# Optimization experiments

Measured on AMD Instinct MI355X. Metric: run time of the kernel, lower is better.

The kernel has to match this reference:

```python
import jax, jax.numpy as jnp
import numpy as np

BRIGHT_THRESH = 0.65
SAT_THRESH = 0.15
SMOOTH_K = 15
LAMBDA_L1 = 1.0
LAMBDA_WIN_L1 = 3.0
LAMBDA_WIN_COLOR = 1.0
WINDOW_WEIGHT = 5.0
BASE_WEIGHT = 1.0
TRANSFORM_WEIGHT = 2.0
EPS = 1e-8


def _avg_pool_same(x, k=SMOOTH_K):
    # AvgPool2d(k, stride=1, padding=k//2), count_include_pad=True (torch default)
    p = k // 2
    s = jax.lax.reduce_window(x, 0.0, jax.lax.add, (1, 1, k, k), (1, 1, 1, 1),
                              [(0, 0), (0, 0), (p, p), (p, p)])
    return s / (k * k)


def _window_detector(source):
    # Rescale from [-1,1] to [0,1] if any negative values present
    src = jnp.where(source.min() < 0, (source + 1) * 0.5, source)
    brightness = 0.299 * src[:, 0:1] + 0.587 * src[:, 1:2] + 0.114 * src[:, 2:3]
    bright_mask = jax.nn.sigmoid(20.0 * (brightness - BRIGHT_THRESH))
    saturation = src.max(axis=1, keepdims=True) - src.min(axis=1, keepdims=True)
    low_sat_mask = jax.nn.sigmoid(20.0 * (SAT_THRESH - saturation))
    return _avg_pool_same(bright_mask * low_sat_mask)


def _normalize_ch(x):
    # F.normalize over channel dim with eps clamp
    n = jnp.sqrt(jnp.sum(x * x, axis=1, keepdims=True))
    return x / jnp.maximum(n, EPS)


def setup_inputs() -> dict:
    key = jax.random.key(0)
    k1, k2, k3 = jax.random.split(key, 3)
    shape = (16, 3, 512, 512)
    return {
        "pred": jax.random.normal(k1, shape, dtype=jnp.float32),
        "target": jax.random.normal(k2, shape, dtype=jnp.float32),
        "source": jax.random.normal(k3, shape, dtype=jnp.float32),
    }


def reference(pred, target, source):
    window_mask = _window_detector(source)  # [B,1,H,W]

    # plain L1
    l1_loss = jnp.abs(pred - target).mean()

    # window-weighted L1
    weight_map = BASE_WEIGHT + (WINDOW_WEIGHT - BASE_WEIGHT) * window_mask
    win_l1_loss = (jnp.abs(pred - target) * weight_map).mean()

    # window color-transform loss
    st = target - source  # source -> target direction
    sp = pred - source    # source -> pred direction
    alignment = jnp.sum(_normalize_ch(st) * _normalize_ch(sp), axis=1, keepdims=True)
    st_mag = jnp.sqrt(jnp.sum(st * st, axis=1, keepdims=True))
    sp_mag = jnp.sqrt(jnp.sum(sp * sp, axis=1, keepdims=True))
    mag_loss = jnp.abs(sp_mag / (st_mag + EPS) - 1.0)
    color_loss = TRANSFORM_WEIGHT * (window_mask * (1.0 - alignment + 0.5 * mag_loss)).mean()

    total = LAMBDA_L1 * l1_loss + LAMBDA_WIN_L1 * win_l1_loss + LAMBDA_WIN_COLOR * color_loss
    return total
```

## Files before the change

kernel.cpp:

```cpp
#include <hip/hip_runtime.h>
#include <math.h>

#define W 512
#define H 512
#define BATCH 16
#define HW (W * H)
#define NPIX (BATCH * HW)
#define NELEM (3 * NPIX)

#define TW 64
#define TH 32
#define NBLOCKS 2048

#define MROWS 46
#define MCOLS 80
#define HSTRIDE 68
#define NQUAD (MROWS * 16)
#define NHALO 408

__device__ __forceinline__ float fast_rcp(float x)  { return __builtin_amdgcn_rcpf(x); }
__device__ __forceinline__ float fast_sqrt(float x) { return __builtin_amdgcn_sqrtf(x); }

__device__ __forceinline__ float maskval(float r, float g, float b) {
    const float R = (r + 1.f) * 0.5f;
    const float G = (g + 1.f) * 0.5f;
    const float B = (b + 1.f) * 0.5f;
    const float bright = 0.299f * R + 0.587f * G + 0.114f * B;
    const float sat = fmaxf(R, fmaxf(G, B)) - fminf(R, fminf(G, B));
    const float bm = fast_rcp(1.f + __expf(-20.f * (bright - 0.65f)));
    const float sm = fast_rcp(1.f + __expf(-20.f * (0.15f - sat)));
    return bm * sm;
}

__device__ __forceinline__ float4 maskval4(float4 R4, float4 G4, float4 B4) {
    float4 m;
    m.x = maskval(R4.x, G4.x, B4.x);
    m.y = maskval(R4.y, G4.y, B4.y);
    m.z = maskval(R4.z, G4.z, B4.z);
    m.w = maskval(R4.w, G4.w, B4.w);
    return m;
}

__device__ __forceinline__ void loss4(const float4& pR, const float4& pG, const float4& pB,
                                      const float4& tR, const float4& tG, const float4& tB,
                                      const float4& sR, const float4& sG, const float4& sB,
                                      const float4& Sw, float& sA, float& sAW, float& sC) {
    const float inv225 = 1.f / 225.f;
    const float wm[4] = {Sw.x * inv225, Sw.y * inv225, Sw.z * inv225, Sw.w * inv225};
    const float pr[4] = {pR.x, pR.y, pR.z, pR.w}, pg[4] = {pG.x, pG.y, pG.z, pG.w},
                pb[4] = {pB.x, pB.y, pB.z, pB.w};
    const float tr[4] = {tR.x, tR.y, tR.z, tR.w}, tg[4] = {tG.x, tG.y, tG.z, tG.w},
                tb[4] = {tB.x, tB.y, tB.z, tB.w};
    const float sr[4] = {sR.x, sR.y, sR.z, sR.w}, sg[4] = {sG.x, sG.y, sG.z, sG.w},
                sb[4] = {sB.x, sB.y, sB.z, sB.w};
#pragma unroll
    for (int j = 0; j < 4; ++j) {
        const float a = fabsf(pr[j] - tr[j]) + fabsf(pg[j] - tg[j]) + fabsf(pb[j] - tb[j]);
        const float stx = tr[j] - sr[j], sty = tg[j] - sg[j], stz = tb[j] - sb[j];
        const float spx = pr[j] - sr[j], spy = pg[j] - sg[j], spz = pb[j] - sb[j];
        const float dot = stx * spx + sty * spy + stz * spz;
        const float stm = fast_sqrt(stx * stx + sty * sty + stz * stz);
        const float spm = fast_sqrt(spx * spx + spy * spy + spz * spz);
        const float align = dot * fast_rcp(fmaxf(stm, 1e-8f) * fmaxf(spm, 1e-8f));
        const float mag = fabsf(spm * fast_rcp(stm + 1e-8f) - 1.f);
        const float c = 1.f - align + 0.5f * mag;
        sA  += a;
        sAW += a * wm[j];
        sC  += c * wm[j];
    }
}

__global__ __launch_bounds__(256, 4) void k_fused(const float* __restrict__ pred,
                                                  const float* __restrict__ targ,
                                                  const float* __restrict__ srcp,
                                                  float* __restrict__ partials) {
    __shared__ __align__(16) float buf[MROWS * MCOLS];
    __shared__ float red[3][4];

    const int tid = threadIdx.x;
    const int bid = blockIdx.x;
    const int b  = bid >> 7;
    const int tl = bid & 127;
    const int y0 = (tl >> 3) * TH;
    const int x0 = (tl & 7) * TW;
    const size_t ibase = (size_t)b * 3 * HW;

    const int R = tid >> 4;
    const int q = tid & 15;
    const int yA = y0 + 2 * R;
    const int xq = x0 + 4 * q;
    const size_t base0 = ibase + (size_t)yA * W + xq;
    const size_t base1 = base0 + W;

    const float4 sR0 = *(const float4*)(srcp + base0);
    const float4 sG0 = *(const float4*)(srcp + base0 + HW);
    const float4 sB0 = *(const float4*)(srcp + base0 + 2 * HW);
    const float4 sR1 = *(const float4*)(srcp + base1);
    const float4 sG1 = *(const float4*)(srcp + base1 + HW);
    const float4 sB1 = *(const float4*)(srcp + base1 + 2 * HW);
    const float4 pR0 = *(const float4*)(pred + base0);
    const float4 pG0 = *(const float4*)(pred + base0 + HW);
    const float4 pB0 = *(const float4*)(pred + base0 + 2 * HW);
    const float4 tR0 = *(const float4*)(targ + base0);
    const float4 tG0 = *(const float4*)(targ + base0 + HW);
    const float4 tB0 = *(const float4*)(targ + base0 + 2 * HW);

#pragma unroll
    for (int it = 0; it < 2; ++it) {
        const int hi = it * 256 + tid;
        if (hi < NHALO) {
            int smr, hq;
            if (hi < 280) {
                const int hr = hi / 20;
                smr = (hr < 7) ? hr : hr + 32;
                hq  = hi - hr * 20;
            } else {
                const int j = hi - 280;
                smr = (j >> 2) + 7;
                const int k = j & 3;
                hq  = (k < 2) ? k : k + 16;
            }
            const int gy = y0 - 7 + smr;
            const int gx = x0 - 8 + 4 * hq;
            float4 mv = make_float4(0.f, 0.f, 0.f, 0.f);
            if ((unsigned)gy < (unsigned)H && (unsigned)gx < (unsigned)W) {
                const size_t o = ibase + (size_t)gy * W + gx;
                const float4 R4 = *(const float4*)(srcp + o);
                const float4 G4 = *(const float4*)(srcp + o + HW);
                const float4 B4 = *(const float4*)(srcp + o + 2 * HW);
                mv = maskval4(R4, G4, B4);
            }
            *(float4*)(buf + smr * MCOLS + 4 * hq) = mv;
        }
    }
    *(float4*)(buf + (2 * R + 7) * MCOLS + 8 + 4 * q) = maskval4(sR0, sG0, sB0);
    *(float4*)(buf + (2 * R + 8) * MCOLS + 8 + 4 * q) = maskval4(sR1, sG1, sB1);
    __syncthreads();

    float4 hq3[3];
#pragma unroll
    for (int i = 0; i < 3; ++i) {
        const int p = i * 256 + tid;
        if (p < NQUAD) {
            const int r  = p >> 4;
            const int qq = p & 15;
            const float* mr = buf + r * MCOLS + 4 * qq;
            const float4 v0 = *(const float4*)(mr);
            const float4 v1 = *(const float4*)(mr + 4);
            const float4 v2 = *(const float4*)(mr + 8);
            const float4 v3 = *(const float4*)(mr + 12);
            const float4 v4 = *(const float4*)(mr + 16);
            const float mid = v1.x + v1.y + v1.z + v1.w
                            + v2.x + v2.y + v2.z + v2.w
                            + v3.x + v3.y + v3.z + v3.w;
            float4 h;
            h.x = v0.y + v0.z + v0.w + mid;
            h.y = h.x - v0.y + v4.x;
            h.z = h.y - v0.z + v4.y;
            h.w = h.z - v0.w + v4.z;
            hq3[i] = h;
        }
    }
    __syncthreads();
#pragma unroll
    for (int i = 0; i < 3; ++i) {
        const int p = i * 256 + tid;
        if (p < NQUAD) {
            const int r  = p >> 4;
            const int qq = p & 15;
            *(float4*)(buf + r * HSTRIDE + 4 * qq) = hq3[i];
        }
    }
    __syncthreads();

    const float4 pR1 = *(const float4*)(pred + base1);
    const float4 pG1 = *(const float4*)(pred + base1 + HW);
    const float4 pB1 = *(const float4*)(pred + base1 + 2 * HW);
    const float4 tR1 = *(const float4*)(targ + base1);
    const float4 tG1 = *(const float4*)(targ + base1 + HW);
    const float4 tB1 = *(const float4*)(targ + base1 + 2 * HW);

    const float* hcol = buf + 4 * q;
    float4 S0 = make_float4(0.f, 0.f, 0.f, 0.f);
#pragma unroll
    for (int k = 0; k < 15; ++k) {
        const float4 h = *(const float4*)(hcol + (2 * R + k) * HSTRIDE);
        S0.x += h.x; S0.y += h.y; S0.z += h.z; S0.w += h.w;
    }
    const float4 hsub = *(const float4*)(hcol + (2 * R) * HSTRIDE);
    const float4 hadd = *(const float4*)(hcol + (2 * R + 15) * HSTRIDE);
    const float4 S1 = make_float4(S0.x - hsub.x + hadd.x, S0.y - hsub.y + hadd.y,
                                  S0.z - hsub.z + hadd.z, S0.w - hsub.w + hadd.w);

    float sA = 0.f, sAW = 0.f, sC = 0.f;
    loss4(pR0, pG0, pB0, tR0, tG0, tB0, sR0, sG0, sB0, S0, sA, sAW, sC);
    loss4(pR1, pG1, pB1, tR1, tG1, tB1, sR1, sG1, sB1, S1, sA, sAW, sC);

#pragma unroll
    for (int off = 32; off > 0; off >>= 1) {
        sA  += __shfl_down(sA, off);
        sAW += __shfl_down(sAW, off);
        sC  += __shfl_down(sC, off);
    }
    const int lane = tid & 63;
    const int wave = tid >> 6;
    if (lane == 0) { red[0][wave] = sA; red[1][wave] = sAW; red[2][wave] = sC; }
    __syncthreads();
    if (tid == 0) {
        partials[(size_t)bid * 3 + 0] = red[0][0] + red[0][1] + red[0][2] + red[0][3];
        partials[(size_t)bid * 3 + 1] = red[1][0] + red[1][1] + red[1][2] + red[1][3];
        partials[(size_t)bid * 3 + 2] = red[2][0] + red[2][1] + red[2][2] + red[2][3];
    }
}

__global__ __launch_bounds__(256) void k_final(const float* __restrict__ partials,
                                               float* __restrict__ out) {
    double a = 0.0, aw = 0.0, c = 0.0;
    for (int i = threadIdx.x; i < NBLOCKS; i += 256) {
        a  += (double)partials[(size_t)i * 3 + 0];
        aw += (double)partials[(size_t)i * 3 + 1];
        c  += (double)partials[(size_t)i * 3 + 2];
    }
#pragma unroll
    for (int off = 32; off > 0; off >>= 1) {
        a  += __shfl_down(a, off);
        aw += __shfl_down(aw, off);
        c  += __shfl_down(c, off);
    }
    __shared__ double rd[3][4];
    const int lane = threadIdx.x & 63;
    const int wave = threadIdx.x >> 6;
    if (lane == 0) { rd[0][wave] = a; rd[1][wave] = aw; rd[2][wave] = c; }
    __syncthreads();
    if (threadIdx.x == 0) {
        const double A  = rd[0][0] + rd[0][1] + rd[0][2] + rd[0][3];
        const double AW = rd[1][0] + rd[1][1] + rd[1][2] + rd[1][3];
        const double C  = rd[2][0] + rd[2][1] + rd[2][2] + rd[2][3];
        const double N = (double)NELEM;
        const double M = (double)NPIX;
        out[0] = (float)((4.0 * A + 12.0 * AW) / N + 2.0 * C / M);
    }
}

extern "C" void kernel_launch(void* const* d_in, const int* in_sizes, int n_in,
                              void* d_out, int out_size, void* d_ws, size_t ws_size,
                              hipStream_t stream) {
    const float* pred = (const float*)d_in[0];
    const float* targ = (const float*)d_in[1];
    const float* src  = (const float*)d_in[2];

    float* partials = (float*)d_ws;

    k_fused<<<NBLOCKS, 256, 0, stream>>>(pred, targ, src, partials);
    k_final<<<1, 256, 0, stream>>>(partials, (float*)d_out);
}
```

Baseline: 158.9 us.

## Process two tiles per block with software-prefetched source loads and swizzled block order

Each block now handles two adjacent 64x32 tiles, prefetching the next tile's source and halo into registers while the current tile's box filter runs. Block indices are remapped so that concurrently running blocks are spread across images and tiles. Source values for the loss are reloaded from global memory instead of being kept in registers, which lowers register pressure at the cost of extra loads that should hit in cache. The aim is to hide global load latency behind LDS work, with the trade-off of half as many blocks, more live registers for the prefetch buffers, and an extra barrier per tile.

```diff
diff --git a/kernel.cpp b/kernel.cpp
--- a/kernel.cpp
+++ b/kernel.cpp
@@ -10,7 +10,9 @@
 
 #define TW 64
 #define TH 32
-#define NBLOCKS 2048
+#define TPB 2
+#define NTILES 2048
+#define NBLOCKS (NTILES / TPB)
 
 #define MROWS 46
 #define MCOLS 80
@@ -70,6 +72,35 @@
     }
 }
 
+__device__ __forceinline__ void issue_src(const float* __restrict__ srcp, size_t ibase,
+                                          int y0, int x0, int R, int q,
+                                          const int* hsmr, const int* hqq, const bool* hact,
+                                          float4* c, float4 (*h)[3], bool* hv) {
+    const size_t b0 = ibase + (size_t)(y0 + 2 * R) * W + (x0 + 4 * q);
+    const size_t b1 = b0 + W;
+    c[0] = *(const float4*)(srcp + b0);
+    c[1] = *(const float4*)(srcp + b0 + HW);
+    c[2] = *(const float4*)(srcp + b0 + 2 * HW);
+    c[3] = *(const float4*)(srcp + b1);
+    c[4] = *(const float4*)(srcp + b1 + HW);
+    c[5] = *(const float4*)(srcp + b1 + 2 * HW);
+#pragma unroll
+    for (int it = 0; it < 2; ++it) {
+        hv[it] = false;
+        if (hact[it]) {
+            const int gy = y0 - 7 + hsmr[it];
+            const int gx = x0 - 8 + 4 * hqq[it];
+            if ((unsigned)gy < (unsigned)H && (unsigned)gx < (unsigned)W) {
+                const size_t o = ibase + (size_t)gy * W + gx;
+                h[it][0] = *(const float4*)(srcp + o);
+                h[it][1] = *(const float4*)(srcp + o + HW);
+                h[it][2] = *(const float4*)(srcp + o + 2 * HW);
+                hv[it] = true;
+            }
+        }
+    }
+}
+
 __global__ __launch_bounds__(256, 4) void k_fused(const float* __restrict__ pred,
                                                   const float* __restrict__ targ,
                                                   const float* __restrict__ srcp,
@@ -78,123 +109,158 @@
     __shared__ float red[3][4];
 
     const int tid = threadIdx.x;
-    const int bid = blockIdx.x;
-    const int b  = bid >> 7;
-    const int tl = bid & 127;
-    const int y0 = (tl >> 3) * TH;
-    const int x0 = (tl & 7) * TW;
-    const size_t ibase = (size_t)b * 3 * HW;
+    const int raw = blockIdx.x;
+    const int bid = ((raw & 7) << 7) | (raw >> 3);
+    const int bimg = bid >> 6;
+    const int pr = bid & 63;
+    const size_t ibase = (size_t)bimg * 3 * HW;
 
     const int R = tid >> 4;
     const int q = tid & 15;
-    const int yA = y0 + 2 * R;
-    const int xq = x0 + 4 * q;
-    const size_t base0 = ibase + (size_t)yA * W + xq;
-    const size_t base1 = base0 + W;
-
-    const float4 sR0 = *(const float4*)(srcp + base0);
-    const float4 sG0 = *(const float4*)(srcp + base0 + HW);
-    const float4 sB0 = *(const float4*)(srcp + base0 + 2 * HW);
-    const float4 sR1 = *(const float4*)(srcp + base1);
-    const float4 sG1 = *(const float4*)(srcp + base1 + HW);
-    const float4 sB1 = *(const float4*)(srcp + base1 + 2 * HW);
-    const float4 pR0 = *(const float4*)(pred + base0);
-    const float4 pG0 = *(const float4*)(pred + base0 + HW);
-    const float4 pB0 = *(const float4*)(pred + base0 + 2 * HW);
-    const float4 tR0 = *(const float4*)(targ + base0);
-    const float4 tG0 = *(const float4*)(targ + base0 + HW);
-    const float4 tB0 = *(const float4*)(targ + base0 + 2 * HW);
-
+
+    int hsmr[2], hqq[2];
+    bool hact[2];
 #pragma unroll
     for (int it = 0; it < 2; ++it) {
         const int hi = it * 256 + tid;
-        if (hi < NHALO) {
-            int smr, hq;
-            if (hi < 280) {
-                const int hr = hi / 20;
-                smr = (hr < 7) ? hr : hr + 32;
-                hq  = hi - hr * 20;
-            } else {
-                const int j = hi - 280;
-                smr = (j >> 2) + 7;
-                const int k = j & 3;
-                hq  = (k < 2) ? k : k + 16;
-            }
-            const int gy = y0 - 7 + smr;
-            const int gx = x0 - 8 + 4 * hq;
-            float4 mv = make_float4(0.f, 0.f, 0.f, 0.f);
-            if ((unsigned)gy < (unsigned)H && (unsigned)gx < (unsigned)W) {
-                const size_t o = ibase + (size_t)gy * W + gx;
-                const float4 R4 = *(const float4*)(srcp + o);
-                const float4 G4 = *(const float4*)(srcp + o + HW);
-                const float4 B4 = *(const float4*)(srcp + o + 2 * HW);
-                mv = maskval4(R4, G4, B4);
-            }
-            *(float4*)(buf + smr * MCOLS + 4 * hq) = mv;
-        }
-    }
-    *(float4*)(buf + (2 * R + 7) * MCOLS + 8 + 4 * q) = maskval4(sR0, sG0, sB0);
-    *(float4*)(buf + (2 * R + 8) * MCOLS + 8 + 4 * q) = maskval4(sR1, sG1, sB1);
-    __syncthreads();
-
-    float4 hq3[3];
-#pragma unroll
-    for (int i = 0; i < 3; ++i) {
-        const int p = i * 256 + tid;
-        if (p < NQUAD) {
-            const int r  = p >> 4;
-            const int qq = p & 15;
-            const float* mr = buf + r * MCOLS + 4 * qq;
-            const float4 v0 = *(const float4*)(mr);
-            const float4 v1 = *(const float4*)(mr + 4);
-            const float4 v2 = *(const float4*)(mr + 8);
-            const float4 v3 = *(const float4*)(mr + 12);
-            const float4 v4 = *(const float4*)(mr + 16);
-            const float mid = v1.x + v1.y + v1.z + v1.w
-                            + v2.x + v2.y + v2.z + v2.w
-                            + v3.x + v3.y + v3.z + v3.w;
-            float4 h;
-            h.x = v0.y + v0.z + v0.w + mid;
-            h.y = h.x - v0.y + v4.x;
-            h.z = h.y - v0.z + v4.y;
-            h.w = h.z - v0.w + v4.z;
-            hq3[i] = h;
-        }
-    }
-    __syncthreads();
-#pragma unroll
-    for (int i = 0; i < 3; ++i) {
-        const int p = i * 256 + tid;
-        if (p < NQUAD) {
-            const int r  = p >> 4;
-            const int qq = p & 15;
-            *(float4*)(buf + r * HSTRIDE + 4 * qq) = hq3[i];
-        }
-    }
-    __syncthreads();
-
-    const float4 pR1 = *(const float4*)(pred + base1);
-    const float4 pG1 = *(const float4*)(pred + base1 + HW);
-    const float4 pB1 = *(const float4*)(pred + base1 + 2 * HW);
-    const float4 tR1 = *(const float4*)(targ + base1);
-    const float4 tG1 = *(const float4*)(targ + base1 + HW);
-    const float4 tB1 = *(const float4*)(targ + base1 + 2 * HW);
-
-    const float* hcol = buf + 4 * q;
-    float4 S0 = make_float4(0.f, 0.f, 0.f, 0.f);
-#pragma unroll
-    for (int k = 0; k < 15; ++k) {
-        const float4 h = *(const float4*)(hcol + (2 * R + k) * HSTRIDE);
-        S0.x += h.x; S0.y += h.y; S0.z += h.z; S0.w += h.w;
-    }
-    const float4 hsub = *(const float4*)(hcol + (2 * R) * HSTRIDE);
-    const float4 hadd = *(const float4*)(hcol + (2 * R + 15) * HSTRIDE);
-    const float4 S1 = make_float4(S0.x - hsub.x + hadd.x, S0.y - hsub.y + hadd.y,
-                                  S0.z - hsub.z + hadd.z, S0.w - hsub.w + hadd.w);
+        hact[it] = hi < NHALO;
+        int smr = 0, hq = 0;
+        if (hi < 280) {
+            const int hr = hi / 20;
+            smr = (hr < 7) ? hr : hr + 32;
+            hq  = hi - hr * 20;
+        } else {
+            const int j = hi - 280;
+            smr = (j >> 2) + 7;
+            const int k = j & 3;
+            hq  = (k < 2) ? k : k + 16;
+        }
+        hsmr[it] = smr;
+        hqq[it]  = hq;
+    }
 
     float sA = 0.f, sAW = 0.f, sC = 0.f;
-    loss4(pR0, pG0, pB0, tR0, tG0, tB0, sR0, sG0, sB0, S0, sA, sAW, sC);
-    loss4(pR1, pG1, pB1, tR1, tG1, tB1, sR1, sG1, sB1, S1, sA, sAW, sC);
+
+    float4 c[6], h[2][3];
+    bool hv[2];
+    float4 c2[6], h2[2][3];
+    bool hv2[2];
+    {
+        const int tl0 = 2 * pr;
+        issue_src(srcp, ibase, (tl0 >> 3) * TH, (tl0 & 7) * TW, R, q, hsmr, hqq, hact, c, h, hv);
+    }
+
+#pragma unroll
+    for (int t = 0; t < TPB; ++t) {
+        const int tl = 2 * pr + t;
+        const int y0 = (tl >> 3) * TH;
+        const int x0 = (tl & 7) * TW;
+
+#pragma unroll
+        for (int it = 0; it < 2; ++it) {
+            if (hact[it]) {
+                float4 mv = make_float4(0.f, 0.f, 0.f, 0.f);
+                if (hv[it]) mv = maskval4(h[it][0], h[it][1], h[it][2]);
+                *(float4*)(buf + hsmr[it] * MCOLS + 4 * hqq[it]) = mv;
+            }
+        }
+        *(float4*)(buf + (2 * R + 7) * MCOLS + 8 + 4 * q) = maskval4(c[0], c[1], c[2]);
+        *(float4*)(buf + (2 * R + 8) * MCOLS + 8 + 4 * q) = maskval4(c[3], c[4], c[5]);
+        __syncthreads();
+
+        if (t + 1 < TPB) {
+            const int tl1 = tl + 1;
+            issue_src(srcp, ibase, (tl1 >> 3) * TH, (tl1 & 7) * TW, R, q, hsmr, hqq, hact,
+                      c2, h2, hv2);
+        }
+
+        float4 hq3[3];
+#pragma unroll
+        for (int i = 0; i < 3; ++i) {
+            const int p = i * 256 + tid;
+            if (p < NQUAD) {
+                const int r  = p >> 4;
+                const int qq = p & 15;
+                const float* mr = buf + r * MCOLS + 4 * qq;
+                const float4 v0 = *(const float4*)(mr);
+                const float4 v1 = *(const float4*)(mr + 4);
+                const float4 v2 = *(const float4*)(mr + 8);
+                const float4 v3 = *(const float4*)(mr + 12);
+                const float4 v4 = *(const float4*)(mr + 16);
+                const float mid = v1.x + v1.y + v1.z + v1.w
+                                + v2.x + v2.y + v2.z + v2.w
+                                + v3.x + v3.y + v3.z + v3.w;
+                float4 hh;
+                hh.x = v0.y + v0.z + v0.w + mid;
+                hh.y = hh.x - v0.y + v4.x;
+                hh.z = hh.y - v0.z + v4.y;
+                hh.w = hh.z - v0.w + v4.z;
+                hq3[i] = hh;
+            }
+        }
+        __syncthreads();
+#pragma unroll
+        for (int i = 0; i < 3; ++i) {
+            const int p = i * 256 + tid;
+            if (p < NQUAD) {
+                const int r  = p >> 4;
+                const int qq = p & 15;
+                *(float4*)(buf + r * HSTRIDE + 4 * qq) = hq3[i];
+            }
+        }
+        __syncthreads();
+
+        const size_t b0 = ibase + (size_t)(y0 + 2 * R) * W + (x0 + 4 * q);
+        const size_t b1 = b0 + W;
+
+        const float4 pR0 = *(const float4*)(pred + b0);
+        const float4 pG0 = *(const float4*)(pred + b0 + HW);
+        const float4 pB0 = *(const float4*)(pred + b0 + 2 * HW);
+        const float4 tR0 = *(const float4*)(targ + b0);
+        const float4 tG0 = *(const float4*)(targ + b0 + HW);
+        const float4 tB0 = *(const float4*)(targ + b0 + 2 * HW);
+        const float4 sR0 = *(const float4*)(srcp + b0);
+        const float4 sG0 = *(const float4*)(srcp + b0 + HW);
+        const float4 sB0 = *(const float4*)(srcp + b0 + 2 * HW);
+
+        const float* hcol = buf + 4 * q;
+        float4 S0 = make_float4(0.f, 0.f, 0.f, 0.f);
+#pragma unroll
+        for (int k = 0; k < 15; ++k) {
+            const float4 hh = *(const float4*)(hcol + (2 * R + k) * HSTRIDE);
+            S0.x += hh.x; S0.y += hh.y; S0.z += hh.z; S0.w += hh.w;
+        }
+        const float4 hsub = *(const float4*)(hcol + (2 * R) * HSTRIDE);
+        const float4 hadd = *(const float4*)(hcol + (2 * R + 15) * HSTRIDE);
+        const float4 S1 = make_float4(S0.x - hsub.x + hadd.x, S0.y - hsub.y + hadd.y,
+                                      S0.z - hsub.z + hadd.z, S0.w - hsub.w + hadd.w);
+
+        loss4(pR0, pG0, pB0, tR0, tG0, tB0, sR0, sG0, sB0, S0, sA, sAW, sC);
+
+        const float4 pR1 = *(const float4*)(pred + b1);
+        const float4 pG1 = *(const float4*)(pred + b1 + HW);
+        const float4 pB1 = *(const float4*)(pred + b1 + 2 * HW);
+        const float4 tR1 = *(const float4*)(targ + b1);
+        const float4 tG1 = *(const float4*)(targ + b1 + HW);
+        const float4 tB1 = *(const float4*)(targ + b1 + 2 * HW);
+        const float4 sR1 = *(const float4*)(srcp + b1);
+        const float4 sG1 = *(const float4*)(srcp + b1 + HW);
+        const float4 sB1 = *(const float4*)(srcp + b1 + 2 * HW);
+
+        loss4(pR1, pG1, pB1, tR1, tG1, tB1, sR1, sG1, sB1, S1, sA, sAW, sC);
+
+        __syncthreads();
+
+        if (t + 1 < TPB) {
+#pragma unroll
+            for (int i = 0; i < 6; ++i) c[i] = c2[i];
+#pragma unroll
+            for (int it = 0; it < 2; ++it) {
+                h[it][0] = h2[it][0]; h[it][1] = h2[it][1]; h[it][2] = h2[it][2];
+                hv[it] = hv2[it];
+            }
+        }
+    }
 
 #pragma unroll
     for (int off = 32; off > 0; off >>= 1) {
```

New measurement: 211.9 us. 33.4% more time.

## Give each wavefront its own 64x16 tile to remove block barriers

Applied to the files above, without the earlier changes.

Each wave of a block now handles an independent 64x16 tile with a private LDS region, so the box-filter stages need no __syncthreads and the per-block LDS reduction is replaced by per-wave partial writes. Block indices are swizzled across images, and halo loads are made unconditional by clamping the address and zeroing the result. The cost is a larger halo fraction per tile (30 mask rows for 16 output rows instead of 46 for 32), which means more redundant source loads and sigmoid work, and pred/target loads are issued late. Within a wave, the code relies on lockstep execution for LDS ordering instead of an explicit barrier.

```diff
diff --git a/kernel.cpp b/kernel.cpp
--- a/kernel.cpp
+++ b/kernel.cpp
@@ -8,15 +8,18 @@
 #define NPIX (BATCH * HW)
 #define NELEM (3 * NPIX)
 
-#define TW 64
-#define TH 32
-#define NBLOCKS 2048
-
-#define MROWS 46
-#define MCOLS 80
-#define HSTRIDE 68
-#define NQUAD (MROWS * 16)
-#define NHALO 408
+#define TWT 64
+#define THT 16
+#define NTILES 4096
+#define WPB 4
+#define NBLOCKS (NTILES / WPB)
+
+#define MR 30
+#define MC 80
+#define HS 68
+#define NHQ (MR * 16)
+#define NHALO 344
+#define WLDS (MR * MC)
 
 __device__ __forceinline__ float fast_rcp(float x)  { return __builtin_amdgcn_rcpf(x); }
 __device__ __forceinline__ float fast_sqrt(float x) { return __builtin_amdgcn_sqrtf(x); }
@@ -70,81 +73,96 @@
     }
 }
 
+__device__ __forceinline__ void row_loss(const float* __restrict__ pred,
+                                         const float* __restrict__ targ,
+                                         const float* __restrict__ srcp,
+                                         size_t o, const float4& S,
+                                         float& sA, float& sAW, float& sC) {
+    const float4 pR = *(const float4*)(pred + o);
+    const float4 pG = *(const float4*)(pred + o + HW);
+    const float4 pB = *(const float4*)(pred + o + 2 * HW);
+    const float4 tR = *(const float4*)(targ + o);
+    const float4 tG = *(const float4*)(targ + o + HW);
+    const float4 tB = *(const float4*)(targ + o + 2 * HW);
+    const float4 sR = *(const float4*)(srcp + o);
+    const float4 sG = *(const float4*)(srcp + o + HW);
+    const float4 sB = *(const float4*)(srcp + o + 2 * HW);
+    loss4(pR, pG, pB, tR, tG, tB, sR, sG, sB, S, sA, sAW, sC);
+}
+
 __global__ __launch_bounds__(256, 4) void k_fused(const float* __restrict__ pred,
                                                   const float* __restrict__ targ,
                                                   const float* __restrict__ srcp,
                                                   float* __restrict__ partials) {
-    __shared__ __align__(16) float buf[MROWS * MCOLS];
-    __shared__ float red[3][4];
-
-    const int tid = threadIdx.x;
-    const int bid = blockIdx.x;
-    const int b  = bid >> 7;
-    const int tl = bid & 127;
-    const int y0 = (tl >> 3) * TH;
-    const int x0 = (tl & 7) * TW;
-    const size_t ibase = (size_t)b * 3 * HW;
-
-    const int R = tid >> 4;
-    const int q = tid & 15;
-    const int yA = y0 + 2 * R;
-    const int xq = x0 + 4 * q;
-    const size_t base0 = ibase + (size_t)yA * W + xq;
-    const size_t base1 = base0 + W;
-
-    const float4 sR0 = *(const float4*)(srcp + base0);
-    const float4 sG0 = *(const float4*)(srcp + base0 + HW);
-    const float4 sB0 = *(const float4*)(srcp + base0 + 2 * HW);
-    const float4 sR1 = *(const float4*)(srcp + base1);
-    const float4 sG1 = *(const float4*)(srcp + base1 + HW);
-    const float4 sB1 = *(const float4*)(srcp + base1 + 2 * HW);
-    const float4 pR0 = *(const float4*)(pred + base0);
-    const float4 pG0 = *(const float4*)(pred + base0 + HW);
-    const float4 pB0 = *(const float4*)(pred + base0 + 2 * HW);
-    const float4 tR0 = *(const float4*)(targ + base0);
-    const float4 tG0 = *(const float4*)(targ + base0 + HW);
-    const float4 tB0 = *(const float4*)(targ + base0 + 2 * HW);
-
-#pragma unroll
-    for (int it = 0; it < 2; ++it) {
-        const int hi = it * 256 + tid;
-        if (hi < NHALO) {
+    __shared__ __align__(16) float lds[WPB * WLDS];
+
+    const int tid  = threadIdx.x;
+    const int raw  = blockIdx.x;
+    const int bid  = ((raw & 7) << 7) | (raw >> 3);
+    const int wv   = tid >> 6;
+    const int lane = tid & 63;
+    const int tile = bid * WPB + wv;
+    const int img  = tile >> 8;
+    const int tl   = tile & 255;
+    const int y0   = (tl >> 3) * THT;
+    const int x0   = (tl & 7) * TWT;
+    const size_t ibase = (size_t)img * 3 * HW;
+    float* buf = lds + wv * WLDS;
+
+    const int r4 = lane >> 4;
+    const int q  = lane & 15;
+    const size_t cb = ibase + (size_t)(y0 + 4 * r4) * W + (x0 + 4 * q);
+
+    float4 sr[4], sg[4], sb[4];
+#pragma unroll
+    for (int i = 0; i < 4; ++i) {
+        const size_t o = cb + (size_t)i * W;
+        sr[i] = *(const float4*)(srcp + o);
+        sg[i] = *(const float4*)(srcp + o + HW);
+        sb[i] = *(const float4*)(srcp + o + 2 * HW);
+    }
+
+#pragma unroll
+    for (int it = 0; it < 6; ++it) {
+        const int p = it * 64 + lane;
+        if (p < NHALO) {
             int smr, hq;
-            if (hi < 280) {
-                const int hr = hi / 20;
-                smr = (hr < 7) ? hr : hr + 32;
-                hq  = hi - hr * 20;
+            if (p < 280) {
+                const int hr = p / 20;
+                smr = (hr < 7) ? hr : hr + 16;
+                hq  = p - hr * 20;
             } else {
-                const int j = hi - 280;
+                const int j = p - 280;
                 smr = (j >> 2) + 7;
                 const int k = j & 3;
                 hq  = (k < 2) ? k : k + 16;
             }
             const int gy = y0 - 7 + smr;
             const int gx = x0 - 8 + 4 * hq;
-            float4 mv = make_float4(0.f, 0.f, 0.f, 0.f);
-            if ((unsigned)gy < (unsigned)H && (unsigned)gx < (unsigned)W) {
-                const size_t o = ibase + (size_t)gy * W + gx;
-                const float4 R4 = *(const float4*)(srcp + o);
-                const float4 G4 = *(const float4*)(srcp + o + HW);
-                const float4 B4 = *(const float4*)(srcp + o + 2 * HW);
-                mv = maskval4(R4, G4, B4);
-            }
-            *(float4*)(buf + smr * MCOLS + 4 * hq) = mv;
+            const bool valid = ((unsigned)gy < (unsigned)H) && ((unsigned)gx < (unsigned)W);
+            const size_t o = valid ? (ibase + (size_t)gy * W + gx) : ibase;
+            const float4 A = *(const float4*)(srcp + o);
+            const float4 B = *(const float4*)(srcp + o + HW);
+            const float4 C = *(const float4*)(srcp + o + 2 * HW);
+            float4 mv = maskval4(A, B, C);
+            if (!valid) mv = make_float4(0.f, 0.f, 0.f, 0.f);
+            *(float4*)(buf + smr * MC + 4 * hq) = mv;
         }
     }
-    *(float4*)(buf + (2 * R + 7) * MCOLS + 8 + 4 * q) = maskval4(sR0, sG0, sB0);
-    *(float4*)(buf + (2 * R + 8) * MCOLS + 8 + 4 * q) = maskval4(sR1, sG1, sB1);
-    __syncthreads();
-
-    float4 hq3[3];
-#pragma unroll
-    for (int i = 0; i < 3; ++i) {
-        const int p = i * 256 + tid;
-        if (p < NQUAD) {
+
+#pragma unroll
+    for (int i = 0; i < 4; ++i) {
+        *(float4*)(buf + (7 + 4 * r4 + i) * MC + 8 + 4 * q) = maskval4(sr[i], sg[i], sb[i]);
+    }
+
+    float4 hh[8];
+#pragma unroll
+    for (int i = 0; i < 8; ++i) {
+        const int p = i * 64 + lane;
+        if (p < NHQ) {
             const int r  = p >> 4;
             const int qq = p & 15;
-            const float* mr = buf + r * MCOLS + 4 * qq;
+            const float* mr = buf + r * MC + 4 * qq;
             const float4 v0 = *(const float4*)(mr);
             const float4 v1 = *(const float4*)(mr + 4);
             const float4 v2 = *(const float4*)(mr + 8);
@@ -158,43 +176,50 @@
             h.y = h.x - v0.y + v4.x;
             h.z = h.y - v0.z + v4.y;
             h.w = h.z - v0.w + v4.z;
-            hq3[i] = h;
+            hh[i] = h;
         }
     }
-    __syncthreads();
-#pragma unroll
-    for (int i = 0; i < 3; ++i) {
-        const int p = i * 256 + tid;
-        if (p < NQUAD) {
+#pragma unroll
+    for (int i = 0; i < 8; ++i) {
+        const int p = i * 64 + lane;
+        if (p < NHQ) {
             const int r  = p >> 4;
             const int qq = p & 15;
-            *(float4*)(buf + r * HSTRIDE + 4 * qq) = hq3[i];
+            *(float4*)(buf + r * HS + 4 * qq) = hh[i];
         }
     }
-    __syncthreads();
-
-    const float4 pR1 = *(const float4*)(pred + base1);
-    const float4 pG1 = *(const float4*)(pred + base1 + HW);
-    const float4 pB1 = *(const float4*)(pred + base1 + 2 * HW);
-    const float4 tR1 = *(const float4*)(targ + base1);
-    const float4 tG1 = *(const float4*)(targ + base1 + HW);
-    const float4 tB1 = *(const float4*)(targ + base1 + 2 * HW);
 
     const float* hcol = buf + 4 * q;
-    float4 S0 = make_float4(0.f, 0.f, 0.f, 0.f);
-#pragma unroll
-    for (int k = 0; k < 15; ++k) {
-        const float4 h = *(const float4*)(hcol + (2 * R + k) * HSTRIDE);
-        S0.x += h.x; S0.y += h.y; S0.z += h.z; S0.w += h.w;
-    }
-    const float4 hsub = *(const float4*)(hcol + (2 * R) * HSTRIDE);
-    const float4 hadd = *(const float4*)(hcol + (2 * R + 15) * HSTRIDE);
-    const float4 S1 = make_float4(S0.x - hsub.x + hadd.x, S0.y - hsub.y + hadd.y,
-                                  S0.z - hsub.z + hadd.z, S0.w - hsub.w + hadd.w);
+    const int rb = 4 * r4;
+    const float4 h0 = *(const float4*)(hcol + (rb + 0) * HS);
+    const float4 h1 = *(const float4*)(hcol + (rb + 1) * HS);
+    const float4 h2 = *(const float4*)(hcol + (rb + 2) * HS);
+    float4 S = make_float4(h0.x + h1.x + h2.x, h0.y + h1.y + h2.y,
+                           h0.z + h1.z + h2.z, h0.w + h1.w + h2.w);
+#pragma unroll
+    for (int k = 3; k < 15; ++k) {
+        const float4 hv = *(const float4*)(hcol + (rb + k) * HS);
+        S.x += hv.x; S.y += hv.y; S.z += hv.z; S.w += hv.w;
+    }
 
     float sA = 0.f, sAW = 0.f, sC = 0.f;
-    loss4(pR0, pG0, pB0, tR0, tG0, tB0, sR0, sG0, sB0, S0, sA, sAW, sC);
-    loss4(pR1, pG1, pB1, tR1, tG1, tB1, sR1, sG1, sB1, S1, sA, sAW, sC);
+
+    row_loss(pred, targ, srcp, cb, S, sA, sAW, sC);
+
+    const float4 a15 = *(const float4*)(hcol + (rb + 15) * HS);
+    const float4 S1 = make_float4(S.x - h0.x + a15.x, S.y - h0.y + a15.y,
+                                  S.z - h0.z + a15.z, S.w - h0.w + a15.w);
+    row_loss(pred, targ, srcp, cb + W, S1, sA, sAW, sC);
+
+    const float4 a16 = *(const float4*)(hcol + (rb + 16) * HS);
+    const float4 S2 = make_float4(S1.x - h1.x + a16.x, S1.y - h1.y + a16.y,
+                                  S1.z - h1.z + a16.z, S1.w - h1.w + a16.w);
+    row_loss(pred, targ, srcp, cb + 2 * W, S2, sA, sAW, sC);
+
+    const float4 a17 = *(const float4*)(hcol + (rb + 17) * HS);
+    const float4 S3 = make_float4(S2.x - h2.x + a17.x, S2.y - h2.y + a17.y,
+                                  S2.z - h2.z + a17.z, S2.w - h2.w + a17.w);
+    row_loss(pred, targ, srcp, cb + 3 * W, S3, sA, sAW, sC);
 
 #pragma unroll
     for (int off = 32; off > 0; off >>= 1) {
@@ -202,21 +227,17 @@
         sAW += __shfl_down(sAW, off);
         sC  += __shfl_down(sC, off);
     }
-    const int lane = tid & 63;
-    const int wave = tid >> 6;
-    if (lane == 0) { red[0][wave] = sA; red[1][wave] = sAW; red[2][wave] = sC; }
-    __syncthreads();
-    if (tid == 0) {
-        partials[(size_t)bid * 3 + 0] = red[0][0] + red[0][1] + red[0][2] + red[0][3];
-        partials[(size_t)bid * 3 + 1] = red[1][0] + red[1][1] + red[1][2] + red[1][3];
-        partials[(size_t)bid * 3 + 2] = red[2][0] + red[2][1] + red[2][2] + red[2][3];
+    if (lane == 0) {
+        partials[(size_t)tile * 3 + 0] = sA;
+        partials[(size_t)tile * 3 + 1] = sAW;
+        partials[(size_t)tile * 3 + 2] = sC;
     }
 }
 
 __global__ __launch_bounds__(256) void k_final(const float* __restrict__ partials,
                                                float* __restrict__ out) {
     double a = 0.0, aw = 0.0, c = 0.0;
-    for (int i = threadIdx.x; i < NBLOCKS; i += 256) {
+    for (int i = threadIdx.x; i < NTILES; i += 256) {
         a  += (double)partials[(size_t)i * 3 + 0];
         aw += (double)partials[(size_t)i * 3 + 1];
         c  += (double)partials[(size_t)i * 3 + 2];
```

Result: slower. 192.2 us (+21.0%).

## Fuse final reduction via last-block atomic counter and swizzle block order

Applied to the files above, without the earlier changes.

Replaces the separate final-reduction kernel with a last-block-done pattern: each block publishes its partials with release stores, bumps an atomic counter, and the last block to arrive sums all partials in double precision. It also remaps block indices so consecutive launched blocks hit different batch images (an XCD-aware swizzle), and writes horizontal box sums back in place in shared memory, dropping one barrier and the separate HSTRIDE layout. The aim is to remove the second kernel launch and a barrier, at the cost of a memset launch, atomic traffic and possible LDS bank conflicts from the wider row stride.

```diff
diff --git a/kernel.cpp b/kernel.cpp
--- a/kernel.cpp
+++ b/kernel.cpp
@@ -11,10 +11,10 @@
 #define TW 64
 #define TH 32
 #define NBLOCKS 2048
+#define NTHREADS 256
 
 #define MROWS 46
 #define MCOLS 80
-#define HSTRIDE 68
 #define NQUAD (MROWS * 16)
 #define NHALO 408
 
@@ -70,15 +70,19 @@
     }
 }
 
-__global__ __launch_bounds__(256, 4) void k_fused(const float* __restrict__ pred,
-                                                  const float* __restrict__ targ,
-                                                  const float* __restrict__ srcp,
-                                                  float* __restrict__ partials) {
+__global__ __launch_bounds__(NTHREADS, 4) void k_fused(const float* __restrict__ pred,
+                                                       const float* __restrict__ targ,
+                                                       const float* __restrict__ srcp,
+                                                       unsigned int* __restrict__ counter,
+                                                       float* __restrict__ partials,
+                                                       float* __restrict__ out) {
     __shared__ __align__(16) float buf[MROWS * MCOLS];
     __shared__ float red[3][4];
+    __shared__ int lastflag;
 
     const int tid = threadIdx.x;
-    const int bid = blockIdx.x;
+    const int raw = blockIdx.x;
+    const int bid = ((raw & 7) << 8) | (raw >> 3);
     const int b  = bid >> 7;
     const int tl = bid & 127;
     const int y0 = (tl >> 3) * TH;
@@ -107,7 +111,7 @@
 
 #pragma unroll
     for (int it = 0; it < 2; ++it) {
-        const int hi = it * 256 + tid;
+        const int hi = it * NTHREADS + tid;
         if (hi < NHALO) {
             int smr, hq;
             if (hi < 280) {
@@ -137,14 +141,13 @@
     *(float4*)(buf + (2 * R + 8) * MCOLS + 8 + 4 * q) = maskval4(sR1, sG1, sB1);
     __syncthreads();
 
-    float4 hq3[3];
 #pragma unroll
     for (int i = 0; i < 3; ++i) {
-        const int p = i * 256 + tid;
+        const int p = i * NTHREADS + tid;
         if (p < NQUAD) {
             const int r  = p >> 4;
             const int qq = p & 15;
-            const float* mr = buf + r * MCOLS + 4 * qq;
+            float* mr = buf + r * MCOLS + 4 * qq;
             const float4 v0 = *(const float4*)(mr);
             const float4 v1 = *(const float4*)(mr + 4);
             const float4 v2 = *(const float4*)(mr + 8);
@@ -158,17 +161,7 @@
             h.y = h.x - v0.y + v4.x;
             h.z = h.y - v0.z + v4.y;
             h.w = h.z - v0.w + v4.z;
-            hq3[i] = h;
-        }
-    }
-    __syncthreads();
-#pragma unroll
-    for (int i = 0; i < 3; ++i) {
-        const int p = i * 256 + tid;
-        if (p < NQUAD) {
-            const int r  = p >> 4;
-            const int qq = p & 15;
-            *(float4*)(buf + r * HSTRIDE + 4 * qq) = hq3[i];
+            *(float4*)(mr) = h;
         }
     }
     __syncthreads();
@@ -184,11 +177,11 @@
     float4 S0 = make_float4(0.f, 0.f, 0.f, 0.f);
 #pragma unroll
     for (int k = 0; k < 15; ++k) {
-        const float4 h = *(const float4*)(hcol + (2 * R + k) * HSTRIDE);
+        const float4 h = *(const float4*)(hcol + (2 * R + k) * MCOLS);
         S0.x += h.x; S0.y += h.y; S0.z += h.z; S0.w += h.w;
     }
-    const float4 hsub = *(const float4*)(hcol + (2 * R) * HSTRIDE);
-    const float4 hadd = *(const float4*)(hcol + (2 * R + 15) * HSTRIDE);
+    const float4 hsub = *(const float4*)(hcol + (2 * R) * MCOLS);
+    const float4 hadd = *(const float4*)(hcol + (2 * R + 15) * MCOLS);
     const float4 S1 = make_float4(S0.x - hsub.x + hadd.x, S0.y - hsub.y + hadd.y,
                                   S0.z - hsub.z + hadd.z, S0.w - hsub.w + hadd.w);
 
@@ -206,39 +199,52 @@
     const int wave = tid >> 6;
     if (lane == 0) { red[0][wave] = sA; red[1][wave] = sAW; red[2][wave] = sC; }
     __syncthreads();
+
     if (tid == 0) {
-        partials[(size_t)bid * 3 + 0] = red[0][0] + red[0][1] + red[0][2] + red[0][3];
-        partials[(size_t)bid * 3 + 1] = red[1][0] + red[1][1] + red[1][2] + red[1][3];
-        partials[(size_t)bid * 3 + 2] = red[2][0] + red[2][1] + red[2][2] + red[2][3];
-    }
-}
-
-__global__ __launch_bounds__(256) void k_final(const float* __restrict__ partials,
-                                               float* __restrict__ out) {
-    double a = 0.0, aw = 0.0, c = 0.0;
-    for (int i = threadIdx.x; i < NBLOCKS; i += 256) {
-        a  += (double)partials[(size_t)i * 3 + 0];
-        aw += (double)partials[(size_t)i * 3 + 1];
-        c  += (double)partials[(size_t)i * 3 + 2];
-    }
-#pragma unroll
-    for (int off = 32; off > 0; off >>= 1) {
-        a  += __shfl_down(a, off);
-        aw += __shfl_down(aw, off);
-        c  += __shfl_down(c, off);
-    }
-    __shared__ double rd[3][4];
-    const int lane = threadIdx.x & 63;
-    const int wave = threadIdx.x >> 6;
-    if (lane == 0) { rd[0][wave] = a; rd[1][wave] = aw; rd[2][wave] = c; }
-    __syncthreads();
-    if (threadIdx.x == 0) {
-        const double A  = rd[0][0] + rd[0][1] + rd[0][2] + rd[0][3];
-        const double AW = rd[1][0] + rd[1][1] + rd[1][2] + rd[1][3];
-        const double C  = rd[2][0] + rd[2][1] + rd[2][2] + rd[2][3];
-        const double N = (double)NELEM;
-        const double M = (double)NPIX;
-        out[0] = (float)((4.0 * A + 12.0 * AW) / N + 2.0 * C / M);
+        const float A  = red[0][0] + red[0][1] + red[0][2] + red[0][3];
+        const float AW = red[1][0] + red[1][1] + red[1][2] + red[1][3];
+        const float C  = red[2][0] + red[2][1] + red[2][2] + red[2][3];
+        __hip_atomic_store(&partials[(size_t)bid * 3 + 0], A,  __ATOMIC_RELEASE,
+                           __HIP_MEMORY_SCOPE_AGENT);
+        __hip_atomic_store(&partials[(size_t)bid * 3 + 1], AW, __ATOMIC_RELEASE,
+                           __HIP_MEMORY_SCOPE_AGENT);
+        __hip_atomic_store(&partials[(size_t)bid * 3 + 2], C,  __ATOMIC_RELEASE,
+                           __HIP_MEMORY_SCOPE_AGENT);
+        __threadfence();
+        const unsigned prev = __hip_atomic_fetch_add(counter, 1u, __ATOMIC_ACQ_REL,
+                                                     __HIP_MEMORY_SCOPE_AGENT);
+        lastflag = (prev == (unsigned)(NBLOCKS - 1)) ? 1 : 0;
+    }
+    __syncthreads();
+
+    if (lastflag) {
+        __threadfence();
+        double a = 0.0, aw = 0.0, c = 0.0;
+        for (int i = tid; i < NBLOCKS; i += NTHREADS) {
+            a  += (double)__hip_atomic_load(&partials[(size_t)i * 3 + 0],
+                                            __ATOMIC_RELAXED, __HIP_MEMORY_SCOPE_AGENT);
+            aw += (double)__hip_atomic_load(&partials[(size_t)i * 3 + 1],
+                                            __ATOMIC_RELAXED, __HIP_MEMORY_SCOPE_AGENT);
+            c  += (double)__hip_atomic_load(&partials[(size_t)i * 3 + 2],
+                                            __ATOMIC_RELAXED, __HIP_MEMORY_SCOPE_AGENT);
+        }
+#pragma unroll
+        for (int off = 32; off > 0; off >>= 1) {
+            a  += __shfl_down(a, off);
+            aw += __shfl_down(aw, off);
+            c  += __shfl_down(c, off);
+        }
+        __shared__ double rd[3][4];
+        if (lane == 0) { rd[0][wave] = a; rd[1][wave] = aw; rd[2][wave] = c; }
+        __syncthreads();
+        if (tid == 0) {
+            const double A  = rd[0][0] + rd[0][1] + rd[0][2] + rd[0][3];
+            const double AW = rd[1][0] + rd[1][1] + rd[1][2] + rd[1][3];
+            const double C  = rd[2][0] + rd[2][1] + rd[2][2] + rd[2][3];
+            const double N = (double)NELEM;
+            const double M = (double)NPIX;
+            out[0] = (float)((4.0 * A + 12.0 * AW) / N + 2.0 * C / M);
+        }
     }
 }
 
@@ -249,8 +255,10 @@
     const float* targ = (const float*)d_in[1];
     const float* src  = (const float*)d_in[2];
 
-    float* partials = (float*)d_ws;
-
-    k_fused<<<NBLOCKS, 256, 0, stream>>>(pred, targ, src, partials);
-    k_final<<<1, 256, 0, stream>>>(partials, (float*)d_out);
-}
+    unsigned int* counter = (unsigned int*)d_ws;
+    float* partials = (float*)((char*)d_ws + 16);
+
+    hipMemsetAsync(d_ws, 0, 16, stream);
+    k_fused<<<NBLOCKS, NTHREADS, 0, stream>>>(pred, targ, src, counter, partials,
+                                              (float*)d_out);
+}
```

Result: slower. 536.9 us (+238.0%).
